# Kernel optimization log

Measured on AMD Instinct MI355X. Metric: run time of the kernel, lower is better.

## Reference

```python
import jax, jax.numpy as jnp
import numpy as np

MODEL_DIM = 128
NUM_HEADS = 8

def setup_inputs() -> dict:
    key = jax.random.key(0)
    kx, kq, kk, kv = jax.random.split(key, 4)
    B, S, D, H = 4, 2048, MODEL_DIM, NUM_HEADS
    scale = 1.0 / np.sqrt(D)
    x = jax.random.normal(kx, (B, S, D), dtype=jnp.float32)
    # nn.Linear weights: shape [out_features, in_features] = [H*D, D]
    W_q = jax.random.normal(kq, (H * D, D), dtype=jnp.float32) * scale
    W_k = jax.random.normal(kk, (H * D, D), dtype=jnp.float32) * scale
    W_v = jax.random.normal(kv, (H * D, D), dtype=jnp.float32) * scale
    return {"x": x, "W_q": W_q, "W_k": W_k, "W_v": W_v}

def reference(x, W_q, W_k, W_v):
    B, S, D = x.shape
    H = NUM_HEADS
    # projections: y = x @ W.T, then split heads -> [B, H, S, D]
    def proj(W):
        y = jnp.einsum('bsd,ed->bse', x, W)  # [B, S, H*D]
        return y.reshape(B, S, H, D).transpose(0, 2, 1, 3)
    Q, K, V = proj(W_q), proj(W_k), proj(W_v)
    # scores [B, H, S, S]
    A = jnp.einsum('bhsd,bhtd->bhst', Q, K) / jnp.sqrt(jnp.asarray(D, x.dtype))
    # AV then softmax over the model_dim axis (as in original: softmax after matmul)
    Z = jax.nn.softmax(jnp.einsum('bhst,bhtd->bhsd', A, V), axis=-1)
    return Z
```

## Files before the change

### kernel.cpp

```cpp
#include <hip/hip_runtime.h>
#include <hip/hip_bf16.h>


#define NB 4
#define NS 2048
#define ND 128
#define NH 8
#define EPB (NS * ND)

typedef unsigned short u16;
typedef unsigned int u32;
typedef short bf16x8 __attribute__((ext_vector_type(8)));
typedef float f32x4 __attribute__((ext_vector_type(4)));

struct __align__(8) us4 { u16 a, b, c, d; };

#define MFMA(a, b, c) __builtin_amdgcn_mfma_f32_16x16x32_bf16((a), (b), (c), 0, 0, 0)

__device__ __forceinline__ void splitf(float f, u16& hi, u16& lo) {
    u32 fb = __float_as_uint(f);
    u32 hb = fb + 0x7FFFu + ((fb >> 16) & 1u);
    hi = (u16)(hb >> 16);
    float fh = __uint_as_float((hb >> 16) << 16);
    float fl = f - fh;
    u32 lb = __float_as_uint(fl);
    u32 lr = lb + 0x7FFFu + ((lb >> 16) & 1u);
    lo = (u16)(lr >> 16);
}


__global__ __launch_bounds__(256) void proj_kernel(
    const float* __restrict__ xg, const float* __restrict__ Wqg,
    const float* __restrict__ Wkg, const float* __restrict__ Wvg,
    u16* __restrict__ ws, int b0, int nbh)
{
    __shared__ float xsT[64][68];
    __shared__ float wsT[64][68];

    const int which = blockIdx.z;
    const float* __restrict__ W = (which == 0) ? Wqg : (which == 1) ? Wkg : Wvg;

    const int tid = threadIdx.x;
    const int bgl = blockIdx.x >> 5;
    const int sL0 = (blockIdx.x & 31) * 64;
    const int eL0 = blockIdx.y * 64;
    const int mG0 = (b0 + bgl) * NS + sL0;
    const int tr = tid >> 4;
    const int tc = tid & 15;

    const int fr = tid & 63;
    const int fk = tid >> 6;

    float4 xv[4], wv[4];
    #pragma unroll
    for (int i = 0; i < 4; ++i) {
        xv[i] = *(const float4*)&xg[(size_t)(mG0 + fr) * ND + (fk + i * 4) * 4];
        wv[i] = *(const float4*)&W[(size_t)(eL0 + fr) * ND + (fk + i * 4) * 4];
    }

    float acc[4][4];
    #pragma unroll
    for (int i = 0; i < 4; ++i)
        #pragma unroll
        for (int j = 0; j < 4; ++j) acc[i][j] = 0.f;

    for (int kk = 0; kk < 2; ++kk) {
        __syncthreads();
        #pragma unroll
        for (int i = 0; i < 4; ++i) {
            int kg = fk + i * 4;
            xsT[kg * 4 + 0][fr] = xv[i].x;
            xsT[kg * 4 + 1][fr] = xv[i].y;
            xsT[kg * 4 + 2][fr] = xv[i].z;
            xsT[kg * 4 + 3][fr] = xv[i].w;
            wsT[kg * 4 + 0][fr] = wv[i].x;
            wsT[kg * 4 + 1][fr] = wv[i].y;
            wsT[kg * 4 + 2][fr] = wv[i].z;
            wsT[kg * 4 + 3][fr] = wv[i].w;
        }
        __syncthreads();
        if (kk == 0) {
            #pragma unroll
            for (int i = 0; i < 4; ++i) {
                xv[i] = *(const float4*)&xg[(size_t)(mG0 + fr) * ND + 64 + (fk + i * 4) * 4];
                wv[i] = *(const float4*)&W[(size_t)(eL0 + fr) * ND + 64 + (fk + i * 4) * 4];
            }
        }
        #pragma unroll 4
        for (int k = 0; k < 64; ++k) {
            const float4 a = *(const float4*)&xsT[k][tr * 4];
            const float4 b = *(const float4*)&wsT[k][tc * 4];
            acc[0][0] += a.x * b.x; acc[0][1] += a.x * b.y; acc[0][2] += a.x * b.z; acc[0][3] += a.x * b.w;
            acc[1][0] += a.y * b.x; acc[1][1] += a.y * b.y; acc[1][2] += a.y * b.z; acc[1][3] += a.y * b.w;
            acc[2][0] += a.z * b.x; acc[2][1] += a.z * b.y; acc[2][2] += a.z * b.z; acc[2][3] += a.z * b.w;
            acc[3][0] += a.w * b.x; acc[3][1] += a.w * b.y; acc[3][2] += a.w * b.z; acc[3][3] += a.w * b.w;
        }
    }

    u16 hv[4][4], lv[4][4];
    #pragma unroll
    for (int i = 0; i < 4; ++i)
        #pragma unroll
        for (int j = 0; j < 4; ++j) splitf(acc[i][j], hv[i][j], lv[i][j]);

    const int e0t = eL0 + 4 * tc;
    const int hh  = e0t >> 7;
    const int d0  = e0t & 127;
    const int bhl = bgl * NH + hh;
    const size_t TS = (size_t)nbh * EPB;
    const size_t tb = (size_t)bhl * EPB;

    if (which == 0) {
        u16* HB = ws + 0 * TS + tb;
        u16* LB = ws + 1 * TS + tb;
        const int kc = d0 >> 5, g = (d0 >> 3) & 3, j0 = d0 & 7;
        #pragma unroll
        for (int i = 0; i < 4; ++i) {
            const int s = sL0 + 4 * tr + i;
            const int q16 = s >> 4, c = s & 15;
            size_t flat = ((size_t)(q16 * 4 + kc) * 64 + g * 16 + c) * 8 + j0;
            us4 h4 = { hv[i][0], hv[i][1], hv[i][2], hv[i][3] };
            us4 l4 = { lv[i][0], lv[i][1], lv[i][2], lv[i][3] };
            *(us4*)(HB + flat) = h4;
            *(us4*)(LB + flat) = l4;
        }
    } else if (which == 1) {
        u16* HB = ws + 2 * TS + tb;
        u16* LB = ws + 3 * TS + tb;
        const int kc = d0 >> 5, g = (d0 >> 3) & 3, j0 = d0 & 7;
        #pragma unroll
        for (int i = 0; i < 4; ++i) {
            const int s = sL0 + 4 * tr + i;
            const int T = s >> 5, nt = (s >> 4) & 1, c = s & 15;
            size_t flat = ((size_t)((T * 4 + kc) * 2 + nt) * 64 + g * 16 + c) * 8 + j0;
            us4 h4 = { hv[i][0], hv[i][1], hv[i][2], hv[i][3] };
            us4 l4 = { lv[i][0], lv[i][1], lv[i][2], lv[i][3] };
            *(us4*)(HB + flat) = h4;
            *(us4*)(LB + flat) = l4;
        }
    } else {
        u16* HB = ws + 4 * TS + tb;
        u16* LB = ws + 5 * TS + tb;
        const int s0 = sL0 + 4 * tr;
        const int T = s0 >> 5, gp = (s0 >> 3) & 3, jt0 = s0 & 7;
        #pragma unroll
        for (int j = 0; j < 4; ++j) {
            const int d = d0 + j;
            const int ni = d >> 4, cV = d & 15;
            size_t flat = ((size_t)(T * 8 + ni) * 64 + gp * 16 + cV) * 8 + jt0;
            us4 h4 = { hv[0][j], hv[1][j], hv[2][j], hv[3][j] };
            us4 l4 = { lv[0][j], lv[1][j], lv[2][j], lv[3][j] };
            *(us4*)(HB + flat) = h4;
            *(us4*)(LB + flat) = l4;
        }
    }
}

__global__ __launch_bounds__(256, 2) void attn_kernel(
    const u16* __restrict__ ws, float* __restrict__ outg, int b0, int nbh)
{
    __shared__ __align__(16) u16 sbuf[2][4][4096];
    __shared__ u32 sP[4][32 * 17];

    const int tid = threadIdx.x;
    const int Wv = tid >> 6;
    const int l  = tid & 63;
    const int c  = l & 15;
    const int g  = l >> 4;
    const int bhl = blockIdx.y;
    const size_t tb = (size_t)bhl * EPB;
    const size_t TS = (size_t)nbh * EPB;

    const u16* QH = ws;
    const u16* QL = ws + 1 * TS;
    const u16* KH = ws + 2 * TS;
    const u16* KL = ws + 3 * TS;
    const u16* VH = ws + 4 * TS;
    const u16* VL = ws + 5 * TS;

    const int qb = blockIdx.x * 128 + Wv * 32;

    bf16x8 qh[2][4], ql[2][4];
    #pragma unroll
    for (int mi = 0; mi < 2; ++mi)
        #pragma unroll
        for (int kc = 0; kc < 4; ++kc) {
            size_t f = tb + ((size_t)(((qb + 16 * mi) >> 4) * 4 + kc) * 64 + l) * 8;
            qh[mi][kc] = *(const bf16x8*)(QH + f);
            ql[mi][kc] = *(const bf16x8*)(QL + f);
        }

    f32x4 z[2][8];
    #pragma unroll
    for (int mi = 0; mi < 2; ++mi)
        #pragma unroll
        for (int ni = 0; ni < 8; ++ni) z[mi][ni] = (f32x4){0.f, 0.f, 0.f, 0.f};

    const u16* srcs[4] = { KH, KL, VH, VL };
    auto stage = [&](int buf, int T) {
        #pragma unroll
        for (int t4 = 0; t4 < 4; ++t4)
            #pragma unroll
            for (int r = 0; r < 2; ++r)
                __builtin_amdgcn_global_load_lds(
                    (const __attribute__((address_space(1))) void*)
                        (srcs[t4] + tb + (size_t)T * 4096 + r * 2048 + tid * 8),
                    (__attribute__((address_space(3))) void*)
                        (&sbuf[buf][t4][r * 2048 + tid * 8]),
                    16, 0, 0);
    };

    u32* sPW = &sP[Wv][0];
    const float scale = 0.08838834764831845f;

    stage(0, 0);

    for (int T = 0; T < 64; ++T) {
        const int cur = T & 1;
        if (T < 63) {
            stage(cur ^ 1, T + 1);
            asm volatile("s_waitcnt vmcnt(8)" ::: "memory");
        } else {
            asm volatile("s_waitcnt vmcnt(0)" ::: "memory");
        }
        __builtin_amdgcn_s_barrier();
        asm volatile("" ::: "memory");

        const u16* bKH = &sbuf[cur][0][0];
        const u16* bKL = &sbuf[cur][1][0];
        const u16* bVH = &sbuf[cur][2][0];
        const u16* bVL = &sbuf[cur][3][0];

        f32x4 s[2][2];
        #pragma unroll
        for (int mi = 0; mi < 2; ++mi)
            #pragma unroll
            for (int nt = 0; nt < 2; ++nt) s[mi][nt] = (f32x4){0.f, 0.f, 0.f, 0.f};
        __builtin_amdgcn_s_setprio(1);
        #pragma unroll
        for (int kc = 0; kc < 4; ++kc) {
            bf16x8 kh0 = *(const bf16x8*)(bKH + ((kc * 2 + 0) * 64 + l) * 8);
            bf16x8 kh1 = *(const bf16x8*)(bKH + ((kc * 2 + 1) * 64 + l) * 8);
            bf16x8 kl0 = *(const bf16x8*)(bKL + ((kc * 2 + 0) * 64 + l) * 8);
            bf16x8 kl1 = *(const bf16x8*)(bKL + ((kc * 2 + 1) * 64 + l) * 8);
            #pragma unroll
            for (int mi = 0; mi < 2; ++mi) {
                s[mi][0] = MFMA(qh[mi][kc], kh0, s[mi][0]);
                s[mi][0] = MFMA(qh[mi][kc], kl0, s[mi][0]);
                s[mi][0] = MFMA(ql[mi][kc], kh0, s[mi][0]);
                s[mi][1] = MFMA(qh[mi][kc], kh1, s[mi][1]);
                s[mi][1] = MFMA(qh[mi][kc], kl1, s[mi][1]);
                s[mi][1] = MFMA(ql[mi][kc], kh1, s[mi][1]);
            }
        }
        __builtin_amdgcn_s_setprio(0);

        bf16x8 pa_h[2], pa_l[2];
        #pragma unroll
        for (int mi = 0; mi < 2; ++mi) {
            #pragma unroll
            for (int nt = 0; nt < 2; ++nt)
                #pragma unroll
                for (int r = 0; r < 4; ++r) {
                    float p = s[mi][nt][r] * scale;
                    u16 ph, pl; splitf(p, ph, pl);
                    sPW[(nt * 16 + c) * 17 + 4 * g + r] = (u32)ph | ((u32)pl << 16);
                }
            union { u16 uh[8]; bf16x8 v; } ph8;
            union { u16 ul[8]; bf16x8 v; } pl8;
            #pragma unroll
            for (int j = 0; j < 8; ++j) {
                u32 v = sPW[(8 * g + j) * 17 + c];
                ph8.uh[j] = (u16)(v & 0xFFFFu);
                pl8.ul[j] = (u16)(v >> 16);
            }
            pa_h[mi] = ph8.v;
            pa_l[mi] = pl8.v;
        }

        __builtin_amdgcn_s_setprio(1);
        #pragma unroll
        for (int ni = 0; ni < 8; ++ni) {
            bf16x8 vh = *(const bf16x8*)(bVH + (ni * 64 + l) * 8);
            bf16x8 vl = *(const bf16x8*)(bVL + (ni * 64 + l) * 8);
            #pragma unroll
            for (int mi = 0; mi < 2; ++mi) {
                z[mi][ni] = MFMA(pa_h[mi], vh, z[mi][ni]);
                z[mi][ni] = MFMA(pa_h[mi], vl, z[mi][ni]);
                z[mi][ni] = MFMA(pa_l[mi], vh, z[mi][ni]);
            }
        }
        __builtin_amdgcn_s_setprio(0);

        asm volatile("" ::: "memory");
        __builtin_amdgcn_s_barrier();
    }

    const size_t obase = (size_t)(b0 * NH + bhl) * EPB;
    #pragma unroll
    for (int mi = 0; mi < 2; ++mi)
        #pragma unroll
        for (int r = 0; r < 4; ++r) {
            float v[8];
            float m = -3.4e38f;
            #pragma unroll
            for (int ni = 0; ni < 8; ++ni) { v[ni] = z[mi][ni][r]; m = fmaxf(m, v[ni]); }
            #pragma unroll
            for (int off = 1; off < 16; off <<= 1) m = fmaxf(m, __shfl_xor(m, off, 64));
            float sum = 0.f;
            #pragma unroll
            for (int ni = 0; ni < 8; ++ni) { v[ni] = expf(v[ni] - m); sum += v[ni]; }
            #pragma unroll
            for (int off = 1; off < 16; off <<= 1) sum += __shfl_xor(sum, off, 64);
            const float inv = 1.f / sum;
            const int q = qb + 16 * mi + 4 * g + r;
            #pragma unroll
            for (int ni = 0; ni < 8; ++ni)
                outg[obase + (size_t)q * ND + ni * 16 + c] = v[ni] * inv;
        }
}

extern "C" void kernel_launch(void* const* d_in, const int* in_sizes, int n_in,
                              void* d_out, int out_size, void* d_ws, size_t ws_size,
                              hipStream_t stream)
{
    (void)out_size;
    int xi = 0;
    for (int i = 0; i < n_in && i < 4; ++i)
        if (in_sizes[i] == NB * NS * ND) { xi = i; break; }
    const float* x = (const float*)d_in[xi];
    const float* Wsp[3]; int w = 0;
    for (int i = 0; i < 4; ++i) if (i != xi) Wsp[w++] = (const float*)d_in[i];
    const float* Wq = Wsp[0];
    const float* Wk = Wsp[1];
    const float* Wv = Wsp[2];
    float* out = (float*)d_out;
    u16* ws = (u16*)d_ws;

    auto slice_bytes = [](int nb) { return (size_t)6 * nb * NH * EPB * 2; };
    int nb = (ws_size >= slice_bytes(4)) ? 4 : (ws_size >= slice_bytes(2)) ? 2 : 1;
    const int nbh = nb * NH;

    for (int b0 = 0; b0 < NB; b0 += nb) {
        proj_kernel<<<dim3(nb * 32, 16, 3), dim3(256), 0, stream>>>(
            x, Wq, Wk, Wv, ws, b0, nbh);
        attn_kernel<<<dim3(16, nbh), dim3(256), 0, stream>>>(
            ws, out, b0, nbh);
    }
}
```

Measured before the change: 347.8 us.

## Rewrite projection GEMM with split-bf16 MFMA instead of FP32 FMA

```diff
diff --git a/kernel.cpp b/kernel.cpp
--- a/kernel.cpp
+++ b/kernel.cpp
@@ -12,8 +12,6 @@
 typedef unsigned int u32;
 typedef short bf16x8 __attribute__((ext_vector_type(8)));
 typedef float f32x4 __attribute__((ext_vector_type(4)));
-
-struct __align__(8) us4 { u16 a, b, c, d; };
 
 #define MFMA(a, b, c) __builtin_amdgcn_mfma_f32_16x16x32_bf16((a), (b), (c), 0, 0, 0)
 
@@ -34,126 +32,93 @@
     const float* __restrict__ Wkg, const float* __restrict__ Wvg,
     u16* __restrict__ ws, int b0, int nbh)
 {
-    __shared__ float xsT[64][68];
-    __shared__ float wsT[64][68];
-
     const int which = blockIdx.z;
-    const float* __restrict__ W = (which == 0) ? Wqg : (which == 1) ? Wkg : Wvg;
+    const float* __restrict__ Wt = (which == 0) ? Wqg : (which == 1) ? Wkg : Wvg;
 
     const int tid = threadIdx.x;
-    const int bgl = blockIdx.x >> 5;
-    const int sL0 = (blockIdx.x & 31) * 64;
-    const int eL0 = blockIdx.y * 64;
-    const int mG0 = (b0 + bgl) * NS + sL0;
-    const int tr = tid >> 4;
-    const int tc = tid & 15;
-
-    const int fr = tid & 63;
-    const int fk = tid >> 6;
-
-    float4 xv[4], wv[4];
-    #pragma unroll
-    for (int i = 0; i < 4; ++i) {
-        xv[i] = *(const float4*)&xg[(size_t)(mG0 + fr) * ND + (fk + i * 4) * 4];
-        wv[i] = *(const float4*)&W[(size_t)(eL0 + fr) * ND + (fk + i * 4) * 4];
+    const int wv = tid >> 6;
+    const int l  = tid & 63;
+    const int c  = l & 15;
+    const int g  = l >> 4;
+    const int wr = wv & 1;
+    const int wc = wv >> 1;
+    const int s0 = b0 * NS + blockIdx.x * 64 + wr * 32;
+    const int e0 = blockIdx.y * 128 + wc * 64;
+
+    f32x4 acc[2][4];
+    #pragma unroll
+    for (int mi = 0; mi < 2; ++mi)
+        #pragma unroll
+        for (int ni = 0; ni < 4; ++ni) acc[mi][ni] = (f32x4){0.f, 0.f, 0.f, 0.f};
+
+    #pragma unroll
+    for (int kc = 0; kc < 4; ++kc) {
+        bf16x8 ah[2], al[2], bh[4], bl[4];
+        #pragma unroll
+        for (int mi = 0; mi < 2; ++mi) {
+            const float* p = xg + (size_t)(s0 + mi * 16 + c) * ND + kc * 32 + g * 8;
+            float4 v0 = *(const float4*)p;
+            float4 v1 = *(const float4*)(p + 4);
+            union { u16 u[8]; bf16x8 v; } H, L;
+            float vv[8] = { v0.x, v0.y, v0.z, v0.w, v1.x, v1.y, v1.z, v1.w };
+            #pragma unroll
+            for (int j = 0; j < 8; ++j) splitf(vv[j], H.u[j], L.u[j]);
+            ah[mi] = H.v; al[mi] = L.v;
+        }
+        #pragma unroll
+        for (int ni = 0; ni < 4; ++ni) {
+            const float* p = Wt + (size_t)(e0 + ni * 16 + c) * ND + kc * 32 + g * 8;
+            float4 v0 = *(const float4*)p;
+            float4 v1 = *(const float4*)(p + 4);
+            union { u16 u[8]; bf16x8 v; } H, L;
+            float vv[8] = { v0.x, v0.y, v0.z, v0.w, v1.x, v1.y, v1.z, v1.w };
+            #pragma unroll
+            for (int j = 0; j < 8; ++j) splitf(vv[j], H.u[j], L.u[j]);
+            bh[ni] = H.v; bl[ni] = L.v;
+        }
+        #pragma unroll
+        for (int mi = 0; mi < 2; ++mi)
+            #pragma unroll
+            for (int ni = 0; ni < 4; ++ni) {
+                acc[mi][ni] = MFMA(ah[mi], bh[ni], acc[mi][ni]);
+                acc[mi][ni] = MFMA(ah[mi], bl[ni], acc[mi][ni]);
+                acc[mi][ni] = MFMA(al[mi], bh[ni], acc[mi][ni]);
+            }
     }
 
-    float acc[4][4];
-    #pragma unroll
-    for (int i = 0; i < 4; ++i)
-        #pragma unroll
-        for (int j = 0; j < 4; ++j) acc[i][j] = 0.f;
-
-    for (int kk = 0; kk < 2; ++kk) {
-        __syncthreads();
-        #pragma unroll
-        for (int i = 0; i < 4; ++i) {
-            int kg = fk + i * 4;
-            xsT[kg * 4 + 0][fr] = xv[i].x;
-            xsT[kg * 4 + 1][fr] = xv[i].y;
-            xsT[kg * 4 + 2][fr] = xv[i].z;
-            xsT[kg * 4 + 3][fr] = xv[i].w;
-            wsT[kg * 4 + 0][fr] = wv[i].x;
-            wsT[kg * 4 + 1][fr] = wv[i].y;
-            wsT[kg * 4 + 2][fr] = wv[i].z;
-            wsT[kg * 4 + 3][fr] = wv[i].w;
-        }
-        __syncthreads();
-        if (kk == 0) {
-            #pragma unroll
-            for (int i = 0; i < 4; ++i) {
-                xv[i] = *(const float4*)&xg[(size_t)(mG0 + fr) * ND + 64 + (fk + i * 4) * 4];
-                wv[i] = *(const float4*)&W[(size_t)(eL0 + fr) * ND + 64 + (fk + i * 4) * 4];
-            }
-        }
-        #pragma unroll 4
-        for (int k = 0; k < 64; ++k) {
-            const float4 a = *(const float4*)&xsT[k][tr * 4];
-            const float4 b = *(const float4*)&wsT[k][tc * 4];
-            acc[0][0] += a.x * b.x; acc[0][1] += a.x * b.y; acc[0][2] += a.x * b.z; acc[0][3] += a.x * b.w;
-            acc[1][0] += a.y * b.x; acc[1][1] += a.y * b.y; acc[1][2] += a.y * b.z; acc[1][3] += a.y * b.w;
-            acc[2][0] += a.z * b.x; acc[2][1] += a.z * b.y; acc[2][2] += a.z * b.z; acc[2][3] += a.z * b.w;
-            acc[3][0] += a.w * b.x; acc[3][1] += a.w * b.y; acc[3][2] += a.w * b.z; acc[3][3] += a.w * b.w;
-        }
-    }
-
-    u16 hv[4][4], lv[4][4];
-    #pragma unroll
-    for (int i = 0; i < 4; ++i)
-        #pragma unroll
-        for (int j = 0; j < 4; ++j) splitf(acc[i][j], hv[i][j], lv[i][j]);
-
-    const int e0t = eL0 + 4 * tc;
-    const int hh  = e0t >> 7;
-    const int d0  = e0t & 127;
-    const int bhl = bgl * NH + hh;
     const size_t TS = (size_t)nbh * EPB;
-    const size_t tb = (size_t)bhl * EPB;
-
-    if (which == 0) {
-        u16* HB = ws + 0 * TS + tb;
-        u16* LB = ws + 1 * TS + tb;
-        const int kc = d0 >> 5, g = (d0 >> 3) & 3, j0 = d0 & 7;
-        #pragma unroll
-        for (int i = 0; i < 4; ++i) {
-            const int s = sL0 + 4 * tr + i;
-            const int q16 = s >> 4, c = s & 15;
-            size_t flat = ((size_t)(q16 * 4 + kc) * 64 + g * 16 + c) * 8 + j0;
-            us4 h4 = { hv[i][0], hv[i][1], hv[i][2], hv[i][3] };
-            us4 l4 = { lv[i][0], lv[i][1], lv[i][2], lv[i][3] };
-            *(us4*)(HB + flat) = h4;
-            *(us4*)(LB + flat) = l4;
-        }
-    } else if (which == 1) {
-        u16* HB = ws + 2 * TS + tb;
-        u16* LB = ws + 3 * TS + tb;
-        const int kc = d0 >> 5, g = (d0 >> 3) & 3, j0 = d0 & 7;
-        #pragma unroll
-        for (int i = 0; i < 4; ++i) {
-            const int s = sL0 + 4 * tr + i;
-            const int T = s >> 5, nt = (s >> 4) & 1, c = s & 15;
-            size_t flat = ((size_t)((T * 4 + kc) * 2 + nt) * 64 + g * 16 + c) * 8 + j0;
-            us4 h4 = { hv[i][0], hv[i][1], hv[i][2], hv[i][3] };
-            us4 l4 = { lv[i][0], lv[i][1], lv[i][2], lv[i][3] };
-            *(us4*)(HB + flat) = h4;
-            *(us4*)(LB + flat) = l4;
-        }
-    } else {
-        u16* HB = ws + 4 * TS + tb;
-        u16* LB = ws + 5 * TS + tb;
-        const int s0 = sL0 + 4 * tr;
-        const int T = s0 >> 5, gp = (s0 >> 3) & 3, jt0 = s0 & 7;
-        #pragma unroll
-        for (int j = 0; j < 4; ++j) {
-            const int d = d0 + j;
-            const int ni = d >> 4, cV = d & 15;
-            size_t flat = ((size_t)(T * 8 + ni) * 64 + gp * 16 + cV) * 8 + jt0;
-            us4 h4 = { hv[0][j], hv[1][j], hv[2][j], hv[3][j] };
-            us4 l4 = { lv[0][j], lv[1][j], lv[2][j], lv[3][j] };
-            *(us4*)(HB + flat) = h4;
-            *(us4*)(LB + flat) = l4;
-        }
-    }
+    #pragma unroll
+    for (int mi = 0; mi < 2; ++mi)
+        #pragma unroll
+        for (int ni = 0; ni < 4; ++ni)
+            #pragma unroll
+            for (int r = 0; r < 4; ++r) {
+                const int sg = s0 + mi * 16 + 4 * g + r;
+                const int e  = e0 + ni * 16 + c;
+                const int bl_ = (sg >> 11) - b0;
+                const int sl  = sg & 2047;
+                const int h = e >> 7, d = e & 127;
+                const size_t tb = (size_t)(bl_ * NH + h) * EPB;
+                u16 ph, pl;
+                splitf(acc[mi][ni][r], ph, pl);
+                size_t flat;
+                if (which == 0) {
+                    flat = ((size_t)((sl >> 4) * 4 + (d >> 5)) * 64
+                            + ((d >> 3) & 3) * 16 + (sl & 15)) * 8 + (d & 7);
+                    ws[0 * TS + tb + flat] = ph;
+                    ws[1 * TS + tb + flat] = pl;
+                } else if (which == 1) {
+                    flat = ((size_t)(((sl >> 5) * 4 + (d >> 5)) * 2 + ((sl >> 4) & 1)) * 64
+                            + ((d >> 3) & 3) * 16 + (sl & 15)) * 8 + (d & 7);
+                    ws[2 * TS + tb + flat] = ph;
+                    ws[3 * TS + tb + flat] = pl;
+                } else {
+                    flat = ((size_t)((sl >> 5) * 8 + (d >> 4)) * 64
+                            + ((sl >> 3) & 3) * 16 + (d & 15)) * 8 + (sl & 7);
+                    ws[4 * TS + tb + flat] = ph;
+                    ws[5 * TS + tb + flat] = pl;
+                }
+            }
 }
 
 __global__ __launch_bounds__(256, 2) void attn_kernel(
@@ -342,7 +307,7 @@
     const int nbh = nb * NH;
 
     for (int b0 = 0; b0 < NB; b0 += nb) {
-        proj_kernel<<<dim3(nb * 32, 16, 3), dim3(256), 0, stream>>>(
+        proj_kernel<<<dim3(nb * 32, 8, 3), dim3(256), 0, stream>>>(
             x, Wq, Wk, Wv, ws, b0, nbh);
         attn_kernel<<<dim3(16, nbh), dim3(256), 0, stream>>>(
             ws, out, b0, nbh);
```

New measurement: 332.4 us. 4.4% less time.
